# Performance work log

Hardware: AMD Instinct MI355X
Metric: run time of the kernel (lower is better)

## Reference

```python
import jax, jax.numpy as jnp
import numpy as np

NC = 80          # num classes (len(yolov8.names))
CONF = 0.25      # ultralytics conf_thres default
IOU_T = 0.45     # ultralytics iou_thres default
MAX_DET = 300    # module default max_det
K = 1024         # pre-NMS candidate cap (static stand-in for max_nms)
MAX_WH = 7680.0  # ultralytics class-offset for multi-class NMS


def setup_inputs() -> dict:
    key = jax.random.key(0)
    k1, k2, k3 = jax.random.split(key, 3)
    B, A = 32, 8400
    # YOLOv8 head layout: rows 0:4 = xywh (pixels), rows 4: = sigmoid class scores
    xy = jax.random.uniform(k1, (B, 2, A), dtype=jnp.float32) * 640.0
    wh = jax.random.uniform(k2, (B, 2, A), dtype=jnp.float32) * 160.0 + 8.0
    scores = jax.random.uniform(k3, (B, NC, A), dtype=jnp.float32) ** 3  # mostly below conf_thres
    preds = jnp.concatenate([xy, wh, scores], axis=1)  # [B, 4+NC, A]
    return {"preds": preds}


def _box_iou(b):
    # b: [K, 4] xyxy -> [K, K] pairwise IoU
    area = (b[:, 2] - b[:, 0]) * (b[:, 3] - b[:, 1])
    lt = jnp.maximum(b[:, None, :2], b[None, :, :2])
    rb = jnp.minimum(b[:, None, 2:], b[None, :, 2:])
    wh = jnp.clip(rb - lt, 0.0)
    inter = wh[..., 0] * wh[..., 1]
    return inter / (area[:, None] + area[None, :] - inter + 1e-7)


def _nms_single(pred):
    # pred: [4+NC, A]
    boxes_xywh = pred[:4].T           # [A, 4]
    cls_scores = pred[4:].T           # [A, NC]
    conf = cls_scores.max(-1)         # best-class confidence per anchor
    cls = jnp.argmax(cls_scores, -1)
    score = jnp.where(conf > CONF, conf, 0.0)
    top, idx = jax.lax.top_k(score, K)            # K candidates by confidence
    xywh = boxes_xywh[idx]
    half = xywh[:, 2:] * 0.5
    boxes = jnp.concatenate([xywh[:, :2] - half, xywh[:, :2] + half], -1)  # xyxy
    cls_k = cls[idx]
    valid = top > CONF
    # multi-class NMS via per-class coordinate offset (ultralytics trick)
    iou = _box_iou(boxes + (cls_k.astype(boxes.dtype) * MAX_WH)[:, None])
    ar = jnp.arange(K)

    def body(i, st):
        supp, keep = st
        ki = valid[i] & ~supp[i]
        keep = keep.at[i].set(ki)
        supp = supp | (ki & (iou[i] > IOU_T) & (ar > i))
        return supp, keep

    _, keep = jax.lax.fori_loop(0, K, body,
                                (jnp.zeros(K, bool), jnp.zeros(K, bool)))
    fscore = jnp.where(keep, top, 0.0)
    sc, order = jax.lax.top_k(fscore, MAX_DET)
    det = jnp.concatenate(
        [boxes[order], top[order][:, None], cls_k[order].astype(boxes.dtype)[:, None]], -1)
    # pad invalid rows with value NC in every column (matches F.pad(value=len(names)))
    return jnp.where((sc > CONF)[:, None], det, jnp.float32(NC))


def reference(preds):
    # [B, MAX_DET, 6] -> (x1, y1, x2, y2, conf, cls), padded rows filled with NC
    return jax.vmap(_nms_single)(preds)
```

## Files before the change

### kernel.cpp

```cpp
#include <hip/hip_runtime.h>
#include <stdint.h>

typedef unsigned long long u64;
typedef unsigned int u32;

#define NC 80
#define CONF_T 0.25f
#define IOU_THR 0.45f
#define MAX_DET 300
#define KCAND 1024
#define A_ANCH 8400
#define NROWS 84
#define MAX_WH 7680.0f

__global__ __launch_bounds__(512) void yolo_conf_kernel(const float* __restrict__ preds,
                                                        u64* __restrict__ keys) {
    int b = blockIdx.x / 9;
    int g = (blockIdx.x % 9) * 512 + threadIdx.x;
    if (g >= A_ANCH / 2) return;
    int a0 = g * 2;
    const float* base = preds + ((size_t)b * NROWS + 4) * A_ANCH + a0;
    float2 best = *(const float2*)base;
    int bc0 = 0, bc1 = 0;
#pragma unroll 8
    for (int c = 1; c < NC; ++c) {
        float2 v = *(const float2*)(base + (size_t)c * A_ANCH);
        if (v.x > best.x) { best.x = v.x; bc0 = c; }
        if (v.y > best.y) { best.y = v.y; bc1 = c; }
    }
    float s0 = (best.x > CONF_T) ? best.x : 0.0f;
    float s1 = (best.y > CONF_T) ? best.y : 0.0f;
    ulonglong2 kk;
    kk.x = ((u64)__float_as_uint(s0) << 32) | ((u64)(16383 - a0) << 7) | (u64)bc0;
    kk.y = ((u64)__float_as_uint(s1) << 32) | ((u64)(16383 - (a0 + 1)) << 7) | (u64)bc1;
    *(ulonglong2*)(keys + (size_t)b * A_ANCH + a0) = kk;
}

__device__ __forceinline__ float iou_f(float ix1, float iy1, float ix2, float iy2, float iar,
                                       float jx1, float jy1, float jx2, float jy2, float jar) {
    float lx = fmaxf(ix1, jx1), ly = fmaxf(iy1, jy1);
    float rx = fminf(ix2, jx2), ry = fminf(iy2, jy2);
    float ww = fmaxf(__fsub_rn(rx, lx), 0.0f);
    float hh = fmaxf(__fsub_rn(ry, ly), 0.0f);
    float inter = __fmul_rn(ww, hh);
    float den = __fadd_rn(__fsub_rn(__fadd_rn(iar, jar), inter), 1e-7f);
    return __fdiv_rn(inter, den);
}

__device__ __forceinline__ void hadd(u32* h, u32 bin, bool m, int lane) {
    u64 act = __ballot(m);
    if (act == 0) return;
    int fl = __ffsll((unsigned long long)act) - 1;
    u32 fb = __shfl(bin, fl);
    u64 same = __ballot(m && (bin == fb));
    if (lane == fl) atomicAdd(&h[fb], (u32)__popcll(same));
    if (m && (bin != fb)) atomicAdd(&h[bin], 1u);
}

__device__ __forceinline__ u64 bstep(u64 v, u32 idx, u32 size, u32 stride) {
    u64 v2 = __shfl_xor((unsigned long long)v, (int)stride, 64);
    bool keep_big = (((idx & stride) == 0) == ((idx & size) == 0));
    return ((v > v2) == keep_big) ? v : v2;
}

__global__ __launch_bounds__(512) void yolo_nms_kernel(const float* __restrict__ preds,
                                                       const u64* __restrict__ keys,
                                                       float* __restrict__ out) {
    const int b = blockIdx.x;
    const int tid = threadIdx.x;
    const int lane = tid & 63;
    const int wid = tid >> 6;

    __shared__ u32 sc[A_ANCH];
    __shared__ u64 skey[KCAND];
    __shared__ u32 histw[8 * 257];
    __shared__ u32 hist[256];
    union OvU {
        struct { u32 eqw[264]; u32 wpre[264]; } pre;
        struct {
            u64 rows[64];
            int keptlist[364];
            float kx1[364], ky1[364], kx2[364], ky2[364], kar[364];
            u32 kcls[364];
        } post;
    };
    __shared__ OvU ov;
    __shared__ u32 s_scal[4];
    __shared__ u32 s_csupp[2];
    __shared__ u32 s_nkept;

    const u64* kb = keys + (size_t)b * A_ANCH;

    for (int i = tid; i < 8 * 257; i += 512) histw[i] = 0;
    if (tid == 0) { s_scal[0] = 0; s_scal[1] = KCAND; s_scal[2] = 0; s_csupp[0] = 0; s_csupp[1] = 0; s_nkept = 0; }

    u32 vals[17];
#pragma unroll
    for (int it = 0; it < 17; ++it) {
        int a = tid + it * 512;
        vals[it] = (a < A_ANCH) ? (u32)(kb[a] >> 32) : 0u;
    }
#pragma unroll
    for (int it = 0; it < 17; ++it) {
        int a = tid + it * 512;
        if (a < A_ANCH) sc[a] = vals[it];
    }
    __syncthreads();

    u32* hw = histw + wid * 257;
    for (int p = 0; p < 4; ++p) {
        if (p == 0) {
#pragma unroll
            for (int it = 0; it < 17; ++it) {
                int a = tid + it * 512;
                hadd(hw, vals[it] >> 24, a < A_ANCH, lane);
            }
        } else {
            for (int i = tid; i < 8 * 257; i += 512) histw[i] = 0;
            __syncthreads();
            u32 prefix = s_scal[0];
            int shift = 24 - 8 * p;
            for (int it = 0; it < 17; ++it) {
                int a = tid + it * 512;
                u32 v = (a < A_ANCH) ? sc[a] : 0u;
                bool m = (a < A_ANCH) && ((v >> (shift + 8)) == prefix);
                hadd(hw, (v >> shift) & 255u, m, lane);
            }
        }
        __syncthreads();
        if (tid < 256) {
            u32 s = 0;
#pragma unroll
            for (int w = 0; w < 8; ++w) s += histw[w * 257 + tid];
            hist[tid] = s;
        }
        __syncthreads();
        if (wid == 0) {
            u32 g[4], loc = 0;
#pragma unroll
            for (int q = 0; q < 4; ++q) { g[q] = hist[255 - (lane * 4 + q)]; loc += g[q]; }
            u32 pre = loc;
#pragma unroll
            for (int off = 1; off < 64; off <<= 1) {
                u32 o = __shfl_up(pre, off);
                if (lane >= off) pre += o;
            }
            u32 run = pre - loc;
            u32 rem = s_scal[1];
            u32 pfx = s_scal[0];
#pragma unroll
            for (int q = 0; q < 4; ++q) {
                int d = 255 - (lane * 4 + q);
                if (run < rem && rem <= run + g[q]) {
                    s_scal[0] = (pfx << 8) | (u32)d;
                    s_scal[1] = rem - run;
                }
                run += g[q];
            }
        }
        __syncthreads();
    }
    const u32 P = s_scal[0];
    const u32 tEq = s_scal[1];

    if (tid < 264) ov.pre.eqw[tid] = 0;
    __syncthreads();
    for (int it = 0; it < 17; ++it) {
        int a = tid + it * 512;
        if (a < A_ANCH && sc[a] == P) atomicOr(&ov.pre.eqw[a >> 5], 1u << (a & 31));
    }
    __syncthreads();
    if (wid == 0) {
        u32 cnt[5], loc = 0;
#pragma unroll
        for (int q = 0; q < 5; ++q) {
            int w2 = lane * 5 + q;
            u32 e = (w2 < 264) ? ov.pre.eqw[w2] : 0u;
            cnt[q] = (u32)__popc(e); loc += cnt[q];
        }
        u32 pre = loc;
#pragma unroll
        for (int off = 1; off < 64; off <<= 1) {
            u32 o = __shfl_up(pre, off);
            if (lane >= off) pre += o;
        }
        u32 run = pre - loc;
#pragma unroll
        for (int q = 0; q < 5; ++q) {
            int w2 = lane * 5 + q;
            if (w2 < 264) ov.pre.wpre[w2] = run;
            run += cnt[q];
        }
    }
    __syncthreads();

    for (int it = 0; it < 17; ++it) {
        int a = tid + it * 512;
        if (a < A_ANCH) {
            u32 v = sc[a];
            bool take = v > P;
            if (!take && v == P) {
                u32 r = ov.pre.wpre[a >> 5] + (u32)__popc(ov.pre.eqw[a >> 5] & ((1u << (a & 31)) - 1u));
                take = (r < tEq);
            }
            if (take) {
                u32 pos = atomicAdd(&s_scal[2], 1u);
                skey[pos] = kb[a];
            }
        }
    }
    __syncthreads();

    {
        u64 vA = skey[tid], vB = skey[tid + 512];
        const u32 iA = (u32)tid, iB = (u32)tid + 512;
#pragma unroll
        for (u32 size = 2; size <= 64; size <<= 1) {
#pragma unroll
            for (u32 stride = size >> 1; stride >= 1; stride >>= 1) {
                vA = bstep(vA, iA, size, stride);
                vB = bstep(vB, iB, size, stride);
            }
        }
        skey[tid] = vA; skey[tid + 512] = vB;
        __syncthreads();
        for (u32 size = 128; size <= 1024; size <<= 1) {
            for (u32 stride = size >> 1; stride >= 64; stride >>= 1) {
                u32 i1 = ((tid & ~(int)(stride - 1)) << 1) | (tid & (stride - 1));
                u32 i2 = i1 + stride;
                bool desc = ((i1 & size) == 0);
                u64 x = skey[i1], y = skey[i2];
                if ((x < y) == desc) { skey[i1] = y; skey[i2] = x; }
                __syncthreads();
            }
            vA = skey[tid]; vB = skey[tid + 512];
#pragma unroll
            for (u32 stride = 32; stride >= 1; stride >>= 1) {
                vA = bstep(vA, iA, size, stride);
                vB = bstep(vB, iB, size, stride);
            }
            skey[tid] = vA; skey[tid + 512] = vB;
            __syncthreads();
        }
    }

    float* BX1 = (float*)sc;
    float* BY1 = BX1 + KCAND;
    float* BX2 = BX1 + 2 * KCAND;
    float* BY2 = BX1 + 3 * KCAND;
    float* BAR = BX1 + 4 * KCAND;
#pragma unroll
    for (int q = 0; q < 2; ++q) {
        int t = tid + q * 512;
        u64 key = skey[t];
        int cls = (int)(key & 127u);
        int idx = 16383 - (int)((key >> 7) & 16383u);
        const float* pb = preds + (size_t)b * NROWS * A_ANCH + idx;
        float x = pb[0];
        float y = pb[A_ANCH];
        float w = pb[2 * A_ANCH];
        float h = pb[3 * A_ANCH];
        float hw = __fmul_rn(w, 0.5f), hh = __fmul_rn(h, 0.5f);
        float x1 = __fsub_rn(x, hw), x2 = __fadd_rn(x, hw);
        float y1 = __fsub_rn(y, hh), y2 = __fadd_rn(y, hh);
        float off = __fmul_rn((float)cls, MAX_WH);
        float bx1 = __fadd_rn(x1, off), bx2 = __fadd_rn(x2, off);
        float by1 = __fadd_rn(y1, off), by2 = __fadd_rn(y2, off);
        BX1[t] = bx1; BY1[t] = by1; BX2[t] = bx2; BY2[t] = by2;
        BAR[t] = __fmul_rn(__fsub_rn(bx2, bx1), __fsub_rn(by2, by1));
    }
    __syncthreads();

    for (int c = 0; c < KCAND / 64; ++c) {
        int j = c * 64 + lane;
        u64 keyj = skey[j];
        float scj = __uint_as_float((u32)(keyj >> 32));
        u32 clsj = (u32)(keyj & 127u);
        float jx1 = BX1[j], jy1 = BY1[j], jx2 = BX2[j], jy2 = BY2[j], jar = BAR[j];

        u32 nk = s_nkept;
        bool suppbit = false;
        for (u32 k = wid; k < nk; k += 8) {
            bool cm = (ov.post.kcls[k] == clsj);
            if (__ballot(cm)) {
                float iou = iou_f(ov.post.kx1[k], ov.post.ky1[k], ov.post.kx2[k], ov.post.ky2[k],
                                  ov.post.kar[k], jx1, jy1, jx2, jy2, jar);
                suppbit |= (cm && (iou > IOU_THR));
            }
        }
        u64 bm = __ballot(suppbit);
        if (bm && lane == 0) {
            atomicOr(&s_csupp[0], (u32)bm);
            atomicOr(&s_csupp[1], (u32)(bm >> 32));
        }

#pragma unroll
        for (int p2 = 0; p2 < 8; ++p2) {
            int i = p2 * 8 + wid;
            int ci = c * 64 + i;
            u32 clsi = (u32)(skey[ci] & 127u);
            u64 m = 0;
            if (__ballot(clsi == clsj)) {
                float iou = iou_f(BX1[ci], BY1[ci], BX2[ci], BY2[ci], BAR[ci],
                                  jx1, jy1, jx2, jy2, jar);
                m = __ballot((lane > i) && (iou > IOU_THR));
            }
            if (lane == 0) ov.post.rows[i] = m;
        }
        __syncthreads();

        if (wid == 0) {
            u64 row = ov.post.rows[lane];
            u32 rlo = (u32)row, rhi = (u32)(row >> 32);
            u64 csupp = (((u64)s_csupp[1]) << 32) | (u64)s_csupp[0];
            u64 valid = __ballot(scj > CONF_T) & ~csupp;
            u64 supp = 0, keep = 0;
#pragma unroll
            for (int i = 0; i < 64; ++i) {
                u64 ri = (((u64)(u32)__builtin_amdgcn_readlane((int)rhi, i)) << 32) |
                         (u64)(u32)__builtin_amdgcn_readlane((int)rlo, i);
                bool ki = (((valid & ~supp) >> i) & 1ull) != 0;
                if (ki) { keep |= (1ull << i); supp |= ri; }
            }
            u32 base = s_nkept;
            if ((keep >> lane) & 1ull) {
                u32 slot = base + (u32)__popcll(keep & ((1ull << lane) - 1ull));
                ov.post.keptlist[slot] = j;
                ov.post.kx1[slot] = jx1; ov.post.ky1[slot] = jy1;
                ov.post.kx2[slot] = jx2; ov.post.ky2[slot] = jy2;
                ov.post.kar[slot] = jar; ov.post.kcls[slot] = clsj;
            }
            if (lane == 0) {
                s_nkept = base + (u32)__popcll(keep);
                s_csupp[0] = 0; s_csupp[1] = 0;
            }
        }
        __syncthreads();
        if (s_nkept >= MAX_DET) break;
    }

    if (tid < MAX_DET) {
        u32 nk = s_nkept;
        float row[6];
        int t = (tid < (int)(nk < MAX_DET ? nk : MAX_DET)) ? ov.post.keptlist[tid] : -1;
        if (t >= 0) {
            u64 key = skey[t];
            float score = __uint_as_float((u32)(key >> 32));
            int cls = (int)(key & 127u);
            int idx = 16383 - (int)((key >> 7) & 16383u);
            const float* pb = preds + (size_t)b * NROWS * A_ANCH + idx;
            float x = pb[0], y = pb[A_ANCH], w = pb[2 * A_ANCH], h = pb[3 * A_ANCH];
            float hw = __fmul_rn(w, 0.5f), hh = __fmul_rn(h, 0.5f);
            row[0] = __fsub_rn(x, hw);
            row[1] = __fsub_rn(y, hh);
            row[2] = __fadd_rn(x, hw);
            row[3] = __fadd_rn(y, hh);
            row[4] = score;
            row[5] = (float)cls;
        } else {
            row[0] = row[1] = row[2] = row[3] = row[4] = row[5] = (float)NC;
        }
        float* o = out + ((size_t)b * MAX_DET + tid) * 6;
#pragma unroll
        for (int q = 0; q < 6; ++q) o[q] = row[q];
    }
}

extern "C" void kernel_launch(void* const* d_in, const int* in_sizes, int n_in,
                              void* d_out, int out_size, void* d_ws, size_t ws_size,
                              hipStream_t stream) {
    const float* preds = (const float*)d_in[0];
    float* out = (float*)d_out;
    u64* keys = (u64*)d_ws;
    int B = in_sizes[0] / (NROWS * A_ANCH);
    yolo_conf_kernel<<<dim3(B * 9), dim3(512), 0, stream>>>(preds, keys);
    yolo_nms_kernel<<<dim3(B), dim3(512), 0, stream>>>(preds, keys, out);
}
```

Measured before the change: 79.15 us.

## Split monolithic NMS kernel into select, sort and NMS kernels with 12-bit radix

The per-image top-K selection moves into its own 1024-thread kernel. That kernel uses a three-pass radix select with 12/12/8-bit digits instead of four 8-bit passes, and replaces per-wave histograms with direct shared atomics. The bitonic sort and the NMS loop each get their own kernel, and candidates pass between them through global workspace. The aim is fewer radix passes, more threads per image for selection, and lower shared-memory pressure in the NMS kernel. The cost is two extra launches and extra global round-trips, and there are still only 32 blocks per kernel.

```diff
diff --git a/kernel.cpp b/kernel.cpp
--- a/kernel.cpp
+++ b/kernel.cpp
@@ -47,212 +47,212 @@
     return __fdiv_rn(inter, den);
 }
 
-__device__ __forceinline__ void hadd(u32* h, u32 bin, bool m, int lane) {
-    u64 act = __ballot(m);
-    if (act == 0) return;
-    int fl = __ffsll((unsigned long long)act) - 1;
-    u32 fb = __shfl(bin, fl);
-    u64 same = __ballot(m && (bin == fb));
-    if (lane == fl) atomicAdd(&h[fb], (u32)__popcll(same));
-    if (m && (bin != fb)) atomicAdd(&h[bin], 1u);
-}
-
 __device__ __forceinline__ u64 bstep(u64 v, u32 idx, u32 size, u32 stride) {
     u64 v2 = __shfl_xor((unsigned long long)v, (int)stride, 64);
     bool keep_big = (((idx & stride) == 0) == ((idx & size) == 0));
     return ((v > v2) == keep_big) ? v : v2;
 }
 
+__global__ __launch_bounds__(1024) void yolo_select_kernel(const u64* __restrict__ keys,
+                                                           u64* __restrict__ selk) {
+    const int b = blockIdx.x;
+    const int tid = threadIdx.x;
+    const int lane = tid & 63;
+    const int wid = tid >> 6;
+
+    __shared__ u32 sc[A_ANCH];
+    __shared__ u32 hist[4096];
+    __shared__ u32 eqw[264], wpre[264];
+    __shared__ u32 s_scal[4];
+
+    const u64* kb = keys + (size_t)b * A_ANCH;
+    u32 vals[9];
+#pragma unroll
+    for (int it = 0; it < 9; ++it) {
+        int a = tid + it * 1024;
+        vals[it] = (a < A_ANCH) ? (u32)(kb[a] >> 32) : 0u;
+    }
+    for (int i = tid; i < 4096; i += 1024) hist[i] = 0;
+    if (tid == 0) { s_scal[0] = 0; s_scal[1] = KCAND; s_scal[2] = 0; }
+#pragma unroll
+    for (int it = 0; it < 9; ++it) {
+        int a = tid + it * 1024;
+        if (a < A_ANCH) sc[a] = vals[it];
+    }
+    __syncthreads();
+
+#pragma unroll
+    for (int it = 0; it < 9; ++it) {
+        int a = tid + it * 1024;
+        if (a < A_ANCH) atomicAdd(&hist[vals[it] >> 20], 1u);
+    }
+    __syncthreads();
+
+    for (int p = 0; p < 3; ++p) {
+        const int shift = (p == 0) ? 20 : (p == 1) ? 8 : 0;
+        const int nb = (p == 2) ? 256 : 4096;
+        if (wid == 0) {
+            const int per = nb >> 6;
+            const int hi0 = nb - 1 - lane * per;
+            u32 loc = 0;
+            for (int q = 0; q < per; ++q) loc += hist[hi0 - q];
+            u32 pre = loc;
+            for (int off = 1; off < 64; off <<= 1) {
+                u32 o = __shfl_up(pre, off);
+                if (lane >= off) pre += o;
+            }
+            u32 run = pre - loc;
+            u32 rem = s_scal[1], Pk = s_scal[0];
+            for (int q = 0; q < per; ++q) {
+                int d = hi0 - q;
+                u32 g = hist[d];
+                if (run < rem && rem <= run + g) {
+                    s_scal[0] = Pk | ((u32)d << shift);
+                    s_scal[1] = rem - run;
+                }
+                run += g;
+            }
+        }
+        __syncthreads();
+        if (p == 2) break;
+        const int nshift = (p == 0) ? 8 : 0;
+        const u32 nmask = (p == 0) ? 0xFFF00000u : 0xFFFFFF00u;
+        const u32 nbm = (p == 0) ? 4095u : 255u;
+        for (int i = tid; i < 4096; i += 1024) hist[i] = 0;
+        __syncthreads();
+        u32 Pk = s_scal[0];
+#pragma unroll
+        for (int it = 0; it < 9; ++it) {
+            int a = tid + it * 1024;
+            if (a < A_ANCH) {
+                u32 v = sc[a];
+                if ((v & nmask) == Pk) atomicAdd(&hist[(v >> nshift) & nbm], 1u);
+            }
+        }
+        __syncthreads();
+    }
+    const u32 P = s_scal[0];
+    const u32 tEq = s_scal[1];
+
+    if (tid < 264) eqw[tid] = 0;
+    __syncthreads();
+#pragma unroll
+    for (int it = 0; it < 9; ++it) {
+        int a = tid + it * 1024;
+        if (a < A_ANCH && sc[a] == P) atomicOr(&eqw[a >> 5], 1u << (a & 31));
+    }
+    __syncthreads();
+    if (wid == 0) {
+        u32 cnt[5], loc = 0;
+#pragma unroll
+        for (int q = 0; q < 5; ++q) {
+            int w2 = lane * 5 + q;
+            u32 e = (w2 < 264) ? eqw[w2] : 0u;
+            cnt[q] = (u32)__popc(e); loc += cnt[q];
+        }
+        u32 pre = loc;
+#pragma unroll
+        for (int off = 1; off < 64; off <<= 1) {
+            u32 o = __shfl_up(pre, off);
+            if (lane >= off) pre += o;
+        }
+        u32 run = pre - loc;
+#pragma unroll
+        for (int q = 0; q < 5; ++q) {
+            int w2 = lane * 5 + q;
+            if (w2 < 264) wpre[w2] = run;
+            run += cnt[q];
+        }
+    }
+    __syncthreads();
+
+    u64* sout = selk + (size_t)b * KCAND;
+#pragma unroll
+    for (int it = 0; it < 9; ++it) {
+        int a = tid + it * 1024;
+        bool take = false;
+        if (a < A_ANCH) {
+            u32 v = sc[a];
+            take = v > P;
+            if (!take && v == P) {
+                u32 r = wpre[a >> 5] + (u32)__popc(eqw[a >> 5] & ((1u << (a & 31)) - 1u));
+                take = (r < tEq);
+            }
+        }
+        u64 m = __ballot(take);
+        if (m) {
+            int fl = __ffsll((unsigned long long)m) - 1;
+            u32 base = 0;
+            if (lane == fl) base = atomicAdd(&s_scal[2], (u32)__popcll(m));
+            base = __shfl(base, fl);
+            if (take) sout[base + (u32)__popcll(m & ((1ull << lane) - 1ull))] = kb[a];
+        }
+    }
+}
+
+__global__ __launch_bounds__(512) void yolo_sort_kernel(const u64* __restrict__ selk,
+                                                        u64* __restrict__ sortk) {
+    const int b = blockIdx.x;
+    const int tid = threadIdx.x;
+    __shared__ u64 skey[KCAND];
+    const u64* si = selk + (size_t)b * KCAND;
+    u64 vA = si[tid], vB = si[tid + 512];
+    const u32 iA = (u32)tid, iB = (u32)tid + 512;
+#pragma unroll
+    for (u32 size = 2; size <= 64; size <<= 1) {
+#pragma unroll
+        for (u32 stride = size >> 1; stride >= 1; stride >>= 1) {
+            vA = bstep(vA, iA, size, stride);
+            vB = bstep(vB, iB, size, stride);
+        }
+    }
+    skey[tid] = vA; skey[tid + 512] = vB;
+    __syncthreads();
+    for (u32 size = 128; size <= 1024; size <<= 1) {
+        for (u32 stride = size >> 1; stride >= 64; stride >>= 1) {
+            u32 i1 = ((tid & ~(int)(stride - 1)) << 1) | (tid & (stride - 1));
+            u32 i2 = i1 + stride;
+            bool desc = ((i1 & size) == 0);
+            u64 x = skey[i1], y = skey[i2];
+            if ((x < y) == desc) { skey[i1] = y; skey[i2] = x; }
+            __syncthreads();
+        }
+        vA = skey[tid]; vB = skey[tid + 512];
+#pragma unroll
+        for (u32 stride = 32; stride >= 1; stride >>= 1) {
+            vA = bstep(vA, iA, size, stride);
+            vB = bstep(vB, iB, size, stride);
+        }
+        if (size < 1024) { skey[tid] = vA; skey[tid + 512] = vB; __syncthreads(); }
+    }
+    u64* so = sortk + (size_t)b * KCAND;
+    so[tid] = vA; so[tid + 512] = vB;
+}
+
 __global__ __launch_bounds__(512) void yolo_nms_kernel(const float* __restrict__ preds,
-                                                       const u64* __restrict__ keys,
+                                                       const u64* __restrict__ sortk,
                                                        float* __restrict__ out) {
     const int b = blockIdx.x;
     const int tid = threadIdx.x;
     const int lane = tid & 63;
     const int wid = tid >> 6;
 
-    __shared__ u32 sc[A_ANCH];
     __shared__ u64 skey[KCAND];
-    __shared__ u32 histw[8 * 257];
-    __shared__ u32 hist[256];
-    union OvU {
-        struct { u32 eqw[264]; u32 wpre[264]; } pre;
-        struct {
-            u64 rows[64];
-            int keptlist[364];
-            float kx1[364], ky1[364], kx2[364], ky2[364], kar[364];
-            u32 kcls[364];
-        } post;
-    };
-    __shared__ OvU ov;
-    __shared__ u32 s_scal[4];
+    __shared__ float BX1[KCAND], BY1[KCAND], BX2[KCAND], BY2[KCAND], BAR[KCAND];
+    __shared__ u64 rows[64];
+    __shared__ int keptlist[364];
+    __shared__ float kx1[364], ky1[364], kx2[364], ky2[364], kar[364];
+    __shared__ u32 kcls[364];
     __shared__ u32 s_csupp[2];
     __shared__ u32 s_nkept;
 
-    const u64* kb = keys + (size_t)b * A_ANCH;
-
-    for (int i = tid; i < 8 * 257; i += 512) histw[i] = 0;
-    if (tid == 0) { s_scal[0] = 0; s_scal[1] = KCAND; s_scal[2] = 0; s_csupp[0] = 0; s_csupp[1] = 0; s_nkept = 0; }
-
-    u32 vals[17];
-#pragma unroll
-    for (int it = 0; it < 17; ++it) {
-        int a = tid + it * 512;
-        vals[it] = (a < A_ANCH) ? (u32)(kb[a] >> 32) : 0u;
-    }
-#pragma unroll
-    for (int it = 0; it < 17; ++it) {
-        int a = tid + it * 512;
-        if (a < A_ANCH) sc[a] = vals[it];
-    }
-    __syncthreads();
-
-    u32* hw = histw + wid * 257;
-    for (int p = 0; p < 4; ++p) {
-        if (p == 0) {
-#pragma unroll
-            for (int it = 0; it < 17; ++it) {
-                int a = tid + it * 512;
-                hadd(hw, vals[it] >> 24, a < A_ANCH, lane);
-            }
-        } else {
-            for (int i = tid; i < 8 * 257; i += 512) histw[i] = 0;
-            __syncthreads();
-            u32 prefix = s_scal[0];
-            int shift = 24 - 8 * p;
-            for (int it = 0; it < 17; ++it) {
-                int a = tid + it * 512;
-                u32 v = (a < A_ANCH) ? sc[a] : 0u;
-                bool m = (a < A_ANCH) && ((v >> (shift + 8)) == prefix);
-                hadd(hw, (v >> shift) & 255u, m, lane);
-            }
-        }
-        __syncthreads();
-        if (tid < 256) {
-            u32 s = 0;
-#pragma unroll
-            for (int w = 0; w < 8; ++w) s += histw[w * 257 + tid];
-            hist[tid] = s;
-        }
-        __syncthreads();
-        if (wid == 0) {
-            u32 g[4], loc = 0;
-#pragma unroll
-            for (int q = 0; q < 4; ++q) { g[q] = hist[255 - (lane * 4 + q)]; loc += g[q]; }
-            u32 pre = loc;
-#pragma unroll
-            for (int off = 1; off < 64; off <<= 1) {
-                u32 o = __shfl_up(pre, off);
-                if (lane >= off) pre += o;
-            }
-            u32 run = pre - loc;
-            u32 rem = s_scal[1];
-            u32 pfx = s_scal[0];
-#pragma unroll
-            for (int q = 0; q < 4; ++q) {
-                int d = 255 - (lane * 4 + q);
-                if (run < rem && rem <= run + g[q]) {
-                    s_scal[0] = (pfx << 8) | (u32)d;
-                    s_scal[1] = rem - run;
-                }
-                run += g[q];
-            }
-        }
-        __syncthreads();
-    }
-    const u32 P = s_scal[0];
-    const u32 tEq = s_scal[1];
-
-    if (tid < 264) ov.pre.eqw[tid] = 0;
-    __syncthreads();
-    for (int it = 0; it < 17; ++it) {
-        int a = tid + it * 512;
-        if (a < A_ANCH && sc[a] == P) atomicOr(&ov.pre.eqw[a >> 5], 1u << (a & 31));
-    }
-    __syncthreads();
-    if (wid == 0) {
-        u32 cnt[5], loc = 0;
-#pragma unroll
-        for (int q = 0; q < 5; ++q) {
-            int w2 = lane * 5 + q;
-            u32 e = (w2 < 264) ? ov.pre.eqw[w2] : 0u;
-            cnt[q] = (u32)__popc(e); loc += cnt[q];
-        }
-        u32 pre = loc;
-#pragma unroll
-        for (int off = 1; off < 64; off <<= 1) {
-            u32 o = __shfl_up(pre, off);
-            if (lane >= off) pre += o;
-        }
-        u32 run = pre - loc;
-#pragma unroll
-        for (int q = 0; q < 5; ++q) {
-            int w2 = lane * 5 + q;
-            if (w2 < 264) ov.pre.wpre[w2] = run;
-            run += cnt[q];
-        }
-    }
-    __syncthreads();
-
-    for (int it = 0; it < 17; ++it) {
-        int a = tid + it * 512;
-        if (a < A_ANCH) {
-            u32 v = sc[a];
-            bool take = v > P;
-            if (!take && v == P) {
-                u32 r = ov.pre.wpre[a >> 5] + (u32)__popc(ov.pre.eqw[a >> 5] & ((1u << (a & 31)) - 1u));
-                take = (r < tEq);
-            }
-            if (take) {
-                u32 pos = atomicAdd(&s_scal[2], 1u);
-                skey[pos] = kb[a];
-            }
-        }
-    }
-    __syncthreads();
-
-    {
-        u64 vA = skey[tid], vB = skey[tid + 512];
-        const u32 iA = (u32)tid, iB = (u32)tid + 512;
-#pragma unroll
-        for (u32 size = 2; size <= 64; size <<= 1) {
-#pragma unroll
-            for (u32 stride = size >> 1; stride >= 1; stride >>= 1) {
-                vA = bstep(vA, iA, size, stride);
-                vB = bstep(vB, iB, size, stride);
-            }
-        }
-        skey[tid] = vA; skey[tid + 512] = vB;
-        __syncthreads();
-        for (u32 size = 128; size <= 1024; size <<= 1) {
-            for (u32 stride = size >> 1; stride >= 64; stride >>= 1) {
-                u32 i1 = ((tid & ~(int)(stride - 1)) << 1) | (tid & (stride - 1));
-                u32 i2 = i1 + stride;
-                bool desc = ((i1 & size) == 0);
-                u64 x = skey[i1], y = skey[i2];
-                if ((x < y) == desc) { skey[i1] = y; skey[i2] = x; }
-                __syncthreads();
-            }
-            vA = skey[tid]; vB = skey[tid + 512];
-#pragma unroll
-            for (u32 stride = 32; stride >= 1; stride >>= 1) {
-                vA = bstep(vA, iA, size, stride);
-                vB = bstep(vB, iB, size, stride);
-            }
-            skey[tid] = vA; skey[tid + 512] = vB;
-            __syncthreads();
-        }
-    }
-
-    float* BX1 = (float*)sc;
-    float* BY1 = BX1 + KCAND;
-    float* BX2 = BX1 + 2 * KCAND;
-    float* BY2 = BX1 + 3 * KCAND;
-    float* BAR = BX1 + 4 * KCAND;
+    if (tid == 0) { s_csupp[0] = 0; s_csupp[1] = 0; s_nkept = 0; }
+    const u64* so = sortk + (size_t)b * KCAND;
 #pragma unroll
     for (int q = 0; q < 2; ++q) {
         int t = tid + q * 512;
-        u64 key = skey[t];
+        u64 key = so[t];
+        skey[t] = key;
         int cls = (int)(key & 127u);
         int idx = 16383 - (int)((key >> 7) & 16383u);
         const float* pb = preds + (size_t)b * NROWS * A_ANCH + idx;
@@ -281,10 +281,10 @@
         u32 nk = s_nkept;
         bool suppbit = false;
         for (u32 k = wid; k < nk; k += 8) {
-            bool cm = (ov.post.kcls[k] == clsj);
+            bool cm = (kcls[k] == clsj);
             if (__ballot(cm)) {
-                float iou = iou_f(ov.post.kx1[k], ov.post.ky1[k], ov.post.kx2[k], ov.post.ky2[k],
-                                  ov.post.kar[k], jx1, jy1, jx2, jy2, jar);
+                float iou = iou_f(kx1[k], ky1[k], kx2[k], ky2[k], kar[k],
+                                  jx1, jy1, jx2, jy2, jar);
                 suppbit |= (cm && (iou > IOU_THR));
             }
         }
@@ -305,12 +305,12 @@
                                   jx1, jy1, jx2, jy2, jar);
                 m = __ballot((lane > i) && (iou > IOU_THR));
             }
-            if (lane == 0) ov.post.rows[i] = m;
+            if (lane == 0) rows[i] = m;
         }
         __syncthreads();
 
         if (wid == 0) {
-            u64 row = ov.post.rows[lane];
+            u64 row = rows[lane];
             u32 rlo = (u32)row, rhi = (u32)(row >> 32);
             u64 csupp = (((u64)s_csupp[1]) << 32) | (u64)s_csupp[0];
             u64 valid = __ballot(scj > CONF_T) & ~csupp;
@@ -325,10 +325,10 @@
             u32 base = s_nkept;
             if ((keep >> lane) & 1ull) {
                 u32 slot = base + (u32)__popcll(keep & ((1ull << lane) - 1ull));
-                ov.post.keptlist[slot] = j;
-                ov.post.kx1[slot] = jx1; ov.post.ky1[slot] = jy1;
-                ov.post.kx2[slot] = jx2; ov.post.ky2[slot] = jy2;
-                ov.post.kar[slot] = jar; ov.post.kcls[slot] = clsj;
+                keptlist[slot] = j;
+                kx1[slot] = jx1; ky1[slot] = jy1;
+                kx2[slot] = jx2; ky2[slot] = jy2;
+                kar[slot] = jar; kcls[slot] = clsj;
             }
             if (lane == 0) {
                 s_nkept = base + (u32)__popcll(keep);
@@ -342,7 +342,7 @@
     if (tid < MAX_DET) {
         u32 nk = s_nkept;
         float row[6];
-        int t = (tid < (int)(nk < MAX_DET ? nk : MAX_DET)) ? ov.post.keptlist[tid] : -1;
+        int t = (tid < (int)(nk < MAX_DET ? nk : MAX_DET)) ? keptlist[tid] : -1;
         if (t >= 0) {
             u64 key = skey[t];
             float score = __uint_as_float((u32)(key >> 32));
@@ -371,8 +371,12 @@
                               hipStream_t stream) {
     const float* preds = (const float*)d_in[0];
     float* out = (float*)d_out;
+    int B = in_sizes[0] / (NROWS * A_ANCH);
     u64* keys = (u64*)d_ws;
-    int B = in_sizes[0] / (NROWS * A_ANCH);
+    u64* selk = keys + (size_t)B * A_ANCH;
+    u64* sortk = selk + (size_t)B * KCAND;
     yolo_conf_kernel<<<dim3(B * 9), dim3(512), 0, stream>>>(preds, keys);
-    yolo_nms_kernel<<<dim3(B), dim3(512), 0, stream>>>(preds, keys, out);
-}
+    yolo_select_kernel<<<dim3(B), dim3(1024), 0, stream>>>(keys, selk);
+    yolo_sort_kernel<<<dim3(B), dim3(512), 0, stream>>>(selk, sortk);
+    yolo_nms_kernel<<<dim3(B), dim3(512), 0, stream>>>(preds, sortk, out);
+}
```

New measurement: 89.82 us. +13.5%, slower.
